# Kernel tuning notes

Measured on AMD Instinct MI355X. Metric: run time of the kernel, lower is better.

The kernel has to match this reference:

```python
import jax, jax.numpy as jnp
import numpy as np
import math

B, T, C = 8, 2048, 1024
KEY_SIZE, VALUE_SIZE = 1024, 1024


def setup_inputs() -> dict:
    key = jax.random.key(0)
    ks = jax.random.split(key, 7)
    s = 1.0 / math.sqrt(C)
    return {
        "input": jax.random.normal(ks[0], (B, T, C), dtype=jnp.float32),
        "mask": jnp.ones((B, T, 1), dtype=jnp.float32),
        "Wq": jax.random.uniform(ks[1], (C, KEY_SIZE), jnp.float32, -s, s),
        "bq": jax.random.uniform(ks[2], (KEY_SIZE,), jnp.float32, -s, s),
        "Wk": jax.random.uniform(ks[3], (C, KEY_SIZE), jnp.float32, -s, s),
        "bk": jax.random.uniform(ks[4], (KEY_SIZE,), jnp.float32, -s, s),
        "Wv": jax.random.uniform(ks[5], (C, VALUE_SIZE), jnp.float32, -s, s),
        "bv": jax.random.uniform(ks[6], (VALUE_SIZE,), jnp.float32, -s, s),
    }


def reference(input, mask, Wq, bq, Wk, bk, Wv, bv):
    # QKV projections: [B, T, C] @ [C, K] -> [B, T, K]
    query = input @ Wq + bq
    keys = input @ Wk + bk
    values = input @ Wv + bv
    # scores[b, tq, tk] = query[b, tq, :] . keys[b, tk, :]
    scores = jnp.einsum("bqk,btk->bqt", query, keys) / math.sqrt(KEY_SIZE)
    # NOTE: softmax over the QUERY dimension (axis=1), as in the original (dim=1)
    attn = jax.nn.softmax(scores, axis=1)
    out = jnp.einsum("bqt,btv->bqv", attn, values)
    return out * mask
```

## Files before the change

kernel.cpp:

```cpp
#include <hip/hip_runtime.h>
#include <hip/hip_bf16.h>
#include <cstdint>

typedef __attribute__((ext_vector_type(8))) __bf16 bf16x8;
typedef __attribute__((ext_vector_type(4))) float f32x4;
typedef __attribute__((ext_vector_type(8))) unsigned short u16x8;

static __device__ __forceinline__ unsigned short f2b(float f) {
    union { float f; unsigned u; } v; v.f = f;
    unsigned r = v.u + 0x7fffu + ((v.u >> 16) & 1u);
    return (unsigned short)(r >> 16);
}
static __device__ __forceinline__ float b2f(unsigned short b) {
    union { unsigned u; float f; } v; v.u = ((unsigned)b) << 16;
    return v.f;
}

#define LL16(g, l) __builtin_amdgcn_global_load_lds( \
    (const __attribute__((address_space(1))) void*)(g), \
    (__attribute__((address_space(3))) void*)(l), 16, 0, 0)

__global__ void conv_f32_bf16(const float* __restrict__ in,
                              unsigned short* __restrict__ out, long n8) {
    long i = (long)blockIdx.x * blockDim.x + threadIdx.x;
    if (i >= n8) return;
    const float4* p = (const float4*)in + i * 2;
    float4 a = p[0], b = p[1];
    u16x8 r;
    r[0] = f2b(a.x); r[1] = f2b(a.y); r[2] = f2b(a.z); r[3] = f2b(a.w);
    r[4] = f2b(b.x); r[5] = f2b(b.y); r[6] = f2b(b.z); r[7] = f2b(b.w);
    *(u16x8*)(out + i * 8) = r;
}

__global__ void transpose_w(const float* __restrict__ w0,
                            const float* __restrict__ w1,
                            const float* __restrict__ w2,
                            unsigned short* __restrict__ out) {
    __shared__ float tile[32][33];
    int z = blockIdx.z;
    const float* W = (z == 0) ? w0 : (z == 1) ? w1 : w2;
    int n0 = blockIdx.x * 32, c0 = blockIdx.y * 32;
    int tx = threadIdx.x & 31, ty = threadIdx.x >> 5;
    #pragma unroll
    for (int i = 0; i < 32; i += 8)
        tile[ty + i][tx] = W[(long)(c0 + ty + i) * 1024 + n0 + tx];
    __syncthreads();
    unsigned short* o = out + (long)z * 1024 * 1024;
    #pragma unroll
    for (int i = 0; i < 32; i += 8)
        o[(long)(n0 + ty + i) * 1024 + c0 + tx] = f2b(tile[tx][ty + i]);
}

__global__ void scale_vt(unsigned short* __restrict__ Vt,
                         const float* __restrict__ colsum) {
    long i8 = ((long)blockIdx.x * 256 + threadIdx.x) * 8;
    int b = (int)(i8 >> 21);
    int rem = (int)(i8 & ((1 << 21) - 1));
    int t = rem & 2047;
    const float* cs = colsum + b * 2048 + t;
    u16x8 v = *(const u16x8*)(Vt + i8);
    u16x8 o;
    #pragma unroll
    for (int j = 0; j < 8; ++j) o[j] = f2b(b2f(v[j]) / cs[j]);
    *(u16x8*)(Vt + i8) = o;
}


#define BAR() __builtin_amdgcn_s_barrier()
#define WAIT_VM2() asm volatile("s_waitcnt vmcnt(2)" ::: "memory")
#define WAIT_VM0() asm volatile("s_waitcnt vmcnt(0)" ::: "memory")

#define STG_A(buf, h, EOFF) do { \
    LL16(((h) ? sA10 : sA00) + (EOFF), ldsA + (buf)*16384 + (h)*8192 + dst0); \
    LL16(((h) ? sA11 : sA01) + (EOFF), ldsA + (buf)*16384 + (h)*8192 + dst1); } while (0)
#define STG_B(buf, h, EOFF) do { \
    LL16(((h) ? sB10 : sB00) + (EOFF), ldsB + (buf)*16384 + (h)*8192 + dst0); \
    LL16(((h) ? sB11 : sB01) + (EOFF), ldsB + (buf)*16384 + (h)*8192 + dst1); } while (0)

#define LDA(d, mh) do { _Pragma("unroll") for (int fi = 0; fi < 4; ++fi) { \
    af[fi][0] = *(const bf16x8*)(ldsA + (d)*16384 + wr*8192 + baA0 + (mh)*4096 + fi*1024); \
    af[fi][1] = *(const bf16x8*)(ldsA + (d)*16384 + wr*8192 + baA1 + (mh)*4096 + fi*1024); } } while (0)
#define LDB(d, nh, BF) do { _Pragma("unroll") for (int fj = 0; fj < 2; ++fj) { \
    BF[fj][0] = *(const bf16x8*)(ldsB + (d)*16384 + wcH*8192 + baB0 + (nh)*2048 + fj*1024); \
    BF[fj][1] = *(const bf16x8*)(ldsB + (d)*16384 + wcH*8192 + baB1 + (nh)*2048 + fj*1024); } } while (0)

#define MMA(mh, nh, BF) do { \
    __builtin_amdgcn_s_setprio(1); \
    _Pragma("unroll") for (int fi = 0; fi < 4; ++fi) \
    _Pragma("unroll") for (int fj = 0; fj < 2; ++fj) { \
        acc[(mh)*4+fi][(nh)*2+fj] = __builtin_amdgcn_mfma_f32_16x16x32_bf16( \
            af[fi][0], BF[fj][0], acc[(mh)*4+fi][(nh)*2+fj], 0, 0, 0); \
        acc[(mh)*4+fi][(nh)*2+fj] = __builtin_amdgcn_mfma_f32_16x16x32_bf16( \
            af[fi][1], BF[fj][1], acc[(mh)*4+fi][(nh)*2+fj], 0, 0, 0); } \
    __builtin_amdgcn_s_setprio(0); } while (0)

template<int MODE>
__global__ __launch_bounds__(512, 2)
void gemm256(const unsigned short* __restrict__ Aall,
             const unsigned short* __restrict__ Ball,
             void* __restrict__ Cv,
             int M, int N, int K, int ldc,
             long aStride, long bStride, long cStride,
             const float* __restrict__ aux, float* __restrict__ colsum) {
    __shared__ unsigned short lds[65536];
    unsigned short* const ldsA = lds;
    unsigned short* const ldsB = lds + 32768;

    const int gx = gridDim.x, gy = gridDim.y;
    const int nxy = gx * gy;
    const int nwg = nxy * gridDim.z;
    const int orig = (blockIdx.z * gy + blockIdx.y) * gx + blockIdx.x;
    const int swz = (orig & 7) * (nwg >> 3) + (orig >> 3);
    const int bz = swz / nxy;
    const int rem = swz - bz * nxy;
    const int by = rem / gx;
    const int bx = rem - by * gx;

    const unsigned short* A  = Aall + (long)bz * aStride;
    const unsigned short* Bt = Ball + (long)bz * bStride;

    const int tid = threadIdx.x;
    const int lane = tid & 63;
    const int w = tid >> 6;
    const int wr = w >> 2, wc = w & 3;
    const int wcH = wc >> 1;
    const int lr = lane & 15, lg = lane >> 4;

    const int bm = by * 256, bn = bx * 256;
    const int NI = K >> 7;

    const int r0 = tid >> 3;
    const int l0 = (tid & 7) ^ (r0 & 7);
    const unsigned short* sA00 = A  + (long)(bm + r0)       * K + l0 * 8;
    const unsigned short* sA01 = A  + (long)(bm + 64 + r0)  * K + l0 * 8;
    const unsigned short* sA10 = A  + (long)(bm + 128 + r0) * K + l0 * 8;
    const unsigned short* sA11 = A  + (long)(bm + 192 + r0) * K + l0 * 8;
    const unsigned short* sB00 = Bt + (long)(bn + r0)       * K + l0 * 8;
    const unsigned short* sB01 = Bt + (long)(bn + 64 + r0)  * K + l0 * 8;
    const unsigned short* sB10 = Bt + (long)(bn + 128 + r0) * K + l0 * 8;
    const unsigned short* sB11 = Bt + (long)(bn + 192 + r0) * K + l0 * 8;
    const int dst0 = w * 512;
    const int dst1 = 4096 + w * 512;

    const int cx0 = (lg ^ (lr & 7)) * 8;
    const int cx1 = ((4 + lg) ^ (lr & 7)) * 8;
    const int baA0 = lr * 64 + cx0;
    const int baA1 = lr * 64 + cx1;
    const int baB0 = ((wc & 1) * 64 + lr) * 64 + cx0;
    const int baB1 = ((wc & 1) * 64 + lr) * 64 + cx1;

    bf16x8 af[4][2], bfA[2][2], bfB[2][2];
    f32x4 acc[8][4] = {};

    STG_B(0, 0, 0); STG_B(0, 1, 0); STG_A(0, 0, 0); STG_A(0, 1, 0);
    STG_B(1, 0, 64);
    WAIT_VM2();
    BAR();

    for (int i = 0; i < NI; ++i) {
        const bool more = (i + 1 < NI);
        LDA(0, 0); LDB(0, 0, bfA); LDB(0, 1, bfB); STG_B(1, 1, 64);
        BAR(); MMA(0, 0, bfA); BAR();

        STG_A(1, 0, 64);
        BAR(); MMA(0, 1, bfB); BAR();

        LDA(0, 1); STG_A(1, 1, 64);
        BAR(); MMA(1, 1, bfB); BAR();

        if (more) STG_B(0, 0, 128);
        BAR(); MMA(1, 0, bfA);
        if (more) { WAIT_VM2(); } else { WAIT_VM0(); }
        BAR();

        LDA(1, 0); LDB(1, 0, bfA); LDB(1, 1, bfB); if (more) STG_B(0, 1, 128);
        BAR(); MMA(0, 0, bfA); BAR();

        if (more) STG_A(0, 0, 128);
        BAR(); MMA(0, 1, bfB); BAR();

        LDA(1, 1); if (more) STG_A(0, 1, 128);
        BAR(); MMA(1, 1, bfB); BAR();

        if (more) STG_B(1, 0, 192);
        BAR(); MMA(1, 0, bfA);
        WAIT_VM2();
        BAR();

        sA00 += 128; sA01 += 128; sA10 += 128; sA11 += 128;
        sB00 += 128; sB01 += 128; sB10 += 128; sB11 += 128;
    }

    const int rloc0 = wr * 128;
    const int cloc0 = wc * 64;

    if (MODE != 3) {
        unsigned short* C = (unsigned short*)Cv + (long)bz * cStride;
        float* cs = colsum + (long)bz * 2048;
        #pragma unroll
        for (int nj = 0; nj < 4; ++nj) {
            int cl = cloc0 + nj * 16 + lr;
            int cb = cl >> 3, cIn = cl & 7;
            float colB = (MODE == 0) ? aux[bn + cl] : 0.f;
            float psum = 0.f;
            #pragma unroll
            for (int mi = 0; mi < 8; ++mi) {
                #pragma unroll
                for (int r = 0; r < 4; ++r) {
                    int rl = rloc0 + mi * 16 + lg * 4 + r;
                    float v = acc[mi][nj][r];
                    if (MODE == 0) v += colB;
                    else if (MODE == 1) v += aux[bm + rl];
                    else { v = __expf(v * 0.03125f); psum += v; }
                    int ch = cb ^ ((rl & 7) << 2);
                    lds[rl * 256 + ch * 8 + cIn] = f2b(v);
                }
            }
            if (MODE == 2) {
                psum += __shfl_xor(psum, 16);
                psum += __shfl_xor(psum, 32);
                if (lg == 0) atomicAdd(&cs[bn + cl], psum);
            }
        }
        BAR();
        #pragma unroll
        for (int it = 0; it < 16; ++it) {
            int lin = it * 512 + tid;
            int row = lin >> 5;
            int c = lin & 31;
            u16x8 v = *(const u16x8*)&lds[row * 256 + ((c ^ ((row & 7) << 2)) << 3)];
            *(u16x8*)&C[(long)(bm + row) * ldc + bn + c * 8] = v;
        }
    } else {
        float* C = (float*)Cv + (long)bz * cStride;
        const float* mk = aux + (long)bz * 2048;
        float* ft = (float*)lds;
        #pragma unroll
        for (int h = 0; h < 2; ++h) {
            if (h) BAR();
            if (wr == h) {
                #pragma unroll
                for (int nj = 0; nj < 4; ++nj) {
                    int cl = cloc0 + nj * 16 + lr;
                    int cf = cl >> 2, cIn = cl & 3;
                    #pragma unroll
                    for (int mi = 0; mi < 8; ++mi) {
                        #pragma unroll
                        for (int r = 0; r < 4; ++r) {
                            int rl = mi * 16 + lg * 4 + r;
                            float m = mk[bm + h * 128 + rl];
                            int cfs = cf ^ ((rl & 7) << 2);
                            ft[rl * 256 + cfs * 4 + cIn] = acc[mi][nj][r] * m;
                        }
                    }
                }
            }
            BAR();
            #pragma unroll
            for (int it = 0; it < 16; ++it) {
                int lin = it * 512 + tid;
                int row = lin >> 6;
                int cf = lin & 63;
                float4 v = *(const float4*)&ft[row * 256 + ((cf ^ ((row & 7) << 2)) << 2)];
                *(float4*)&C[(long)(bm + h * 128 + row) * ldc + bn + cf * 4] = v;
            }
        }
    }
}

extern "C" void kernel_launch(void* const* d_in, const int* in_sizes, int n_in,
                              void* d_out, int out_size, void* d_ws, size_t ws_size,
                              hipStream_t stream) {
    const float* x    = (const float*)d_in[0];
    const float* mask = (const float*)d_in[1];
    const float* Wq   = (const float*)d_in[2];
    const float* bq   = (const float*)d_in[3];
    const float* Wk   = (const float*)d_in[4];
    const float* bk   = (const float*)d_in[5];
    const float* Wv   = (const float*)d_in[6];
    const float* bv   = (const float*)d_in[7];
    float* out = (float*)d_out;

    const long MT = 16384;
    unsigned short* Xb = (unsigned short*)d_ws;
    unsigned short* Wt = Xb + MT * 1024;
    unsigned short* Q  = Wt + 3L * 1024 * 1024;
    unsigned short* Kk = Q  + MT * 1024;
    unsigned short* Vt = Kk + MT * 1024;
    unsigned short* E  = Vt + 8L * 1024 * 2048;
    float* colsum = (float*)(E + 8L * 2048 * 2048);
    size_t need = (size_t)((char*)(colsum + 8 * 2048) - (char*)d_ws);
    if (ws_size < need) return;

    conv_f32_bf16<<<(MT * 1024) / 8 / 256, 256, 0, stream>>>(x, Xb, (MT * 1024) / 8);
    transpose_w<<<dim3(32, 32, 3), 256, 0, stream>>>(Wq, Wk, Wv, Wt);
    gemm256<0><<<dim3(4, 64, 1), 512, 0, stream>>>(
        Xb, Wt, Q, 16384, 1024, 1024, 1024, 0, 0, 0, bq, nullptr);
    gemm256<0><<<dim3(4, 64, 1), 512, 0, stream>>>(
        Xb, Wt + 1048576, Kk, 16384, 1024, 1024, 1024, 0, 0, 0, bk, nullptr);
    gemm256<1><<<dim3(8, 4, 8), 512, 0, stream>>>(
        Wt + 2097152, Xb, Vt, 1024, 2048, 1024, 2048,
        0, 2048L * 1024, 1024L * 2048, bv, nullptr);
    hipMemsetAsync(colsum, 0, 8 * 2048 * sizeof(float), stream);
    gemm256<2><<<dim3(8, 8, 8), 512, 0, stream>>>(
        Q, Kk, E, 2048, 2048, 1024, 2048,
        2048L * 1024, 2048L * 1024, 2048L * 2048, nullptr, colsum);
    scale_vt<<<8192, 256, 0, stream>>>(Vt, colsum);
    gemm256<3><<<dim3(4, 8, 8), 512, 0, stream>>>(
        E, Vt, out, 2048, 1024, 2048, 1024,
        2048L * 2048, 1024L * 2048, 2048L * 1024, mask, nullptr);
}
```

Measured before the change: 309.9 us.

## Restructure GEMM main loop to overlap LDS reads with MFMA and cut barriers

```diff
diff --git a/kernel.cpp b/kernel.cpp
--- a/kernel.cpp
+++ b/kernel.cpp
@@ -68,6 +68,7 @@
 
 #define BAR() __builtin_amdgcn_s_barrier()
 #define WAIT_VM2() asm volatile("s_waitcnt vmcnt(2)" ::: "memory")
+#define WAIT_VM1() asm volatile("s_waitcnt vmcnt(1)" ::: "memory")
 #define WAIT_VM0() asm volatile("s_waitcnt vmcnt(0)" ::: "memory")
 
 #define STG_A(buf, h, EOFF) do { \
@@ -152,39 +153,35 @@
     bf16x8 af[4][2], bfA[2][2], bfB[2][2];
     f32x4 acc[8][4] = {};
 
-    STG_B(0, 0, 0); STG_B(0, 1, 0); STG_A(0, 0, 0); STG_A(0, 1, 0);
-    STG_B(1, 0, 64);
-    WAIT_VM2();
+    STG_A(0, 0, 0); STG_A(0, 1, 0);
+    STG_B(0, 0, 0); STG_B(0, 1, 0);
+    STG_B(1, 0, 64); STG_B(1, 1, 64);
+    WAIT_VM0();
     BAR();
+    LDA(0, 0);
+    LDB(0, 0, bfA);
+    LDB(0, 1, bfB);
 
     for (int i = 0; i < NI; ++i) {
         const bool more = (i + 1 < NI);
-        LDA(0, 0); LDB(0, 0, bfA); LDB(0, 1, bfB); STG_B(1, 1, 64);
-        BAR(); MMA(0, 0, bfA); BAR();
-
-        STG_A(1, 0, 64);
-        BAR(); MMA(0, 1, bfB); BAR();
-
-        LDA(0, 1); STG_A(1, 1, 64);
-        BAR(); MMA(1, 1, bfB); BAR();
-
-        if (more) STG_B(0, 0, 128);
-        BAR(); MMA(1, 0, bfA);
-        if (more) { WAIT_VM2(); } else { WAIT_VM0(); }
-        BAR();
-
-        LDA(1, 0); LDB(1, 0, bfA); LDB(1, 1, bfB); if (more) STG_B(0, 1, 128);
-        BAR(); MMA(0, 0, bfA); BAR();
-
-        if (more) STG_A(0, 0, 128);
-        BAR(); MMA(0, 1, bfB); BAR();
-
-        LDA(1, 1); if (more) STG_A(0, 1, 128);
-        BAR(); MMA(1, 1, bfB); BAR();
-
-        if (more) STG_B(1, 0, 192);
-        BAR(); MMA(1, 0, bfA);
-        WAIT_VM2();
+        MMA(0, 0, bfA); STG_A(1, 0, 64);
+        BAR();
+        MMA(0, 1, bfB); LDA(0, 1); STG_A(1, 1, 64);
+        WAIT_VM2(); BAR();
+        MMA(1, 1, bfB); LDB(1, 1, bfB); if (more) STG_B(0, 0, 128);
+        if (more) { WAIT_VM1(); } else { WAIT_VM0(); }
+        BAR();
+        MMA(1, 0, bfA); LDB(1, 0, bfA); LDA(1, 0); if (more) STG_B(0, 1, 128);
+        BAR();
+
+        MMA(0, 0, bfA); if (more) STG_A(0, 0, 128);
+        BAR();
+        MMA(0, 1, bfB); LDA(1, 1); if (more) STG_A(0, 1, 128);
+        WAIT_VM2(); BAR();
+        MMA(1, 1, bfB); if (more) { LDB(0, 1, bfB); STG_B(1, 0, 192); }
+        if (more) { WAIT_VM1(); } else { WAIT_VM0(); }
+        BAR();
+        MMA(1, 0, bfA); if (more) { LDB(0, 0, bfA); LDA(0, 0); STG_B(1, 1, 192); }
         BAR();
 
         sA00 += 128; sA01 += 128; sA10 += 128; sA11 += 128;
```

New measurement: 303.9 us. No clear change (-1.9%).

## Replace 256x256 GEMM tile with 256x128 tile using 32x32 MFMA

Applied to the files above, without the earlier changes.

```diff
diff --git a/kernel.cpp b/kernel.cpp
--- a/kernel.cpp
+++ b/kernel.cpp
@@ -3,7 +3,7 @@
 #include <cstdint>
 
 typedef __attribute__((ext_vector_type(8))) __bf16 bf16x8;
-typedef __attribute__((ext_vector_type(4))) float f32x4;
+typedef __attribute__((ext_vector_type(16))) float f32x16;
 typedef __attribute__((ext_vector_type(8))) unsigned short u16x8;
 
 static __device__ __forceinline__ unsigned short f2b(float f) {
@@ -19,6 +19,9 @@
 #define LL16(g, l) __builtin_amdgcn_global_load_lds( \
     (const __attribute__((address_space(1))) void*)(g), \
     (__attribute__((address_space(3))) void*)(l), 16, 0, 0)
+
+#define BAR() __builtin_amdgcn_s_barrier()
+#define WAIT_VM0() asm volatile("s_waitcnt vmcnt(0)" ::: "memory")
 
 __global__ void conv_f32_bf16(const float* __restrict__ in,
                               unsigned short* __restrict__ out, long n8) {
@@ -66,45 +69,17 @@
 }
 
 
-#define BAR() __builtin_amdgcn_s_barrier()
-#define WAIT_VM2() asm volatile("s_waitcnt vmcnt(2)" ::: "memory")
-#define WAIT_VM0() asm volatile("s_waitcnt vmcnt(0)" ::: "memory")
-
-#define STG_A(buf, h, EOFF) do { \
-    LL16(((h) ? sA10 : sA00) + (EOFF), ldsA + (buf)*16384 + (h)*8192 + dst0); \
-    LL16(((h) ? sA11 : sA01) + (EOFF), ldsA + (buf)*16384 + (h)*8192 + dst1); } while (0)
-#define STG_B(buf, h, EOFF) do { \
-    LL16(((h) ? sB10 : sB00) + (EOFF), ldsB + (buf)*16384 + (h)*8192 + dst0); \
-    LL16(((h) ? sB11 : sB01) + (EOFF), ldsB + (buf)*16384 + (h)*8192 + dst1); } while (0)
-
-#define LDA(d, mh) do { _Pragma("unroll") for (int fi = 0; fi < 4; ++fi) { \
-    af[fi][0] = *(const bf16x8*)(ldsA + (d)*16384 + wr*8192 + baA0 + (mh)*4096 + fi*1024); \
-    af[fi][1] = *(const bf16x8*)(ldsA + (d)*16384 + wr*8192 + baA1 + (mh)*4096 + fi*1024); } } while (0)
-#define LDB(d, nh, BF) do { _Pragma("unroll") for (int fj = 0; fj < 2; ++fj) { \
-    BF[fj][0] = *(const bf16x8*)(ldsB + (d)*16384 + wcH*8192 + baB0 + (nh)*2048 + fj*1024); \
-    BF[fj][1] = *(const bf16x8*)(ldsB + (d)*16384 + wcH*8192 + baB1 + (nh)*2048 + fj*1024); } } while (0)
-
-#define MMA(mh, nh, BF) do { \
-    __builtin_amdgcn_s_setprio(1); \
-    _Pragma("unroll") for (int fi = 0; fi < 4; ++fi) \
-    _Pragma("unroll") for (int fj = 0; fj < 2; ++fj) { \
-        acc[(mh)*4+fi][(nh)*2+fj] = __builtin_amdgcn_mfma_f32_16x16x32_bf16( \
-            af[fi][0], BF[fj][0], acc[(mh)*4+fi][(nh)*2+fj], 0, 0, 0); \
-        acc[(mh)*4+fi][(nh)*2+fj] = __builtin_amdgcn_mfma_f32_16x16x32_bf16( \
-            af[fi][1], BF[fj][1], acc[(mh)*4+fi][(nh)*2+fj], 0, 0, 0); } \
-    __builtin_amdgcn_s_setprio(0); } while (0)
-
 template<int MODE>
-__global__ __launch_bounds__(512, 2)
-void gemm256(const unsigned short* __restrict__ Aall,
+__global__ __launch_bounds__(512, 4)
+void gemm128(const unsigned short* __restrict__ Aall,
              const unsigned short* __restrict__ Ball,
              void* __restrict__ Cv,
              int M, int N, int K, int ldc,
              long aStride, long bStride, long cStride,
              const float* __restrict__ aux, float* __restrict__ colsum) {
-    __shared__ unsigned short lds[65536];
+    __shared__ unsigned short lds[32768];
     unsigned short* const ldsA = lds;
-    unsigned short* const ldsB = lds + 32768;
+    unsigned short* const ldsB = lds + 16384;
 
     const int gx = gridDim.x, gy = gridDim.y;
     const int nxy = gx * gy;
@@ -122,113 +97,98 @@
     const int tid = threadIdx.x;
     const int lane = tid & 63;
     const int w = tid >> 6;
-    const int wr = w >> 2, wc = w & 3;
-    const int wcH = wc >> 1;
-    const int lr = lane & 15, lg = lane >> 4;
-
-    const int bm = by * 256, bn = bx * 256;
-    const int NI = K >> 7;
-
-    const int r0 = tid >> 3;
-    const int l0 = (tid & 7) ^ (r0 & 7);
-    const unsigned short* sA00 = A  + (long)(bm + r0)       * K + l0 * 8;
-    const unsigned short* sA01 = A  + (long)(bm + 64 + r0)  * K + l0 * 8;
-    const unsigned short* sA10 = A  + (long)(bm + 128 + r0) * K + l0 * 8;
-    const unsigned short* sA11 = A  + (long)(bm + 192 + r0) * K + l0 * 8;
-    const unsigned short* sB00 = Bt + (long)(bn + r0)       * K + l0 * 8;
-    const unsigned short* sB01 = Bt + (long)(bn + 64 + r0)  * K + l0 * 8;
-    const unsigned short* sB10 = Bt + (long)(bn + 128 + r0) * K + l0 * 8;
-    const unsigned short* sB11 = Bt + (long)(bn + 192 + r0) * K + l0 * 8;
-    const int dst0 = w * 512;
-    const int dst1 = 4096 + w * 512;
-
-    const int cx0 = (lg ^ (lr & 7)) * 8;
-    const int cx1 = ((4 + lg) ^ (lr & 7)) * 8;
-    const int baA0 = lr * 64 + cx0;
-    const int baA1 = lr * 64 + cx1;
-    const int baB0 = ((wc & 1) * 64 + lr) * 64 + cx0;
-    const int baB1 = ((wc & 1) * 64 + lr) * 64 + cx1;
-
-    bf16x8 af[4][2], bfA[2][2], bfB[2][2];
-    f32x4 acc[8][4] = {};
-
-    STG_B(0, 0, 0); STG_B(0, 1, 0); STG_A(0, 0, 0); STG_A(0, 1, 0);
-    STG_B(1, 0, 64);
-    WAIT_VM2();
+    const int wrow = w >> 1, wcol = w & 1;
+    const int l31 = lane & 31, hi = lane >> 5;
+
+    const int bm = by * 256, bn = bx * 128;
+    const int NT = K >> 5;
+
+    const int r0 = tid >> 2;
+    const int c0 = (tid & 3) ^ (r0 & 3);
+    const unsigned short* sA0 = A  + (long)(bm + r0)       * K + c0 * 8;
+    const unsigned short* sA1 = A  + (long)(bm + 128 + r0) * K + c0 * 8;
+    const unsigned short* sB0 = Bt + (long)(bn + r0)       * K + c0 * 8;
+    const int dA0 = w * 512;
+    const int dA1 = 4096 + w * 512;
+    const int dB0 = w * 512;
+
+    const int s3 = l31 & 3;
+    const int cx0 = ((0 + hi) ^ s3) * 8;
+    const int cx1 = ((2 + hi) ^ s3) * 8;
+    const int baA = (wrow * 64 + l31) * 32;
+    const int baB = (wcol * 64 + l31) * 32;
+
+    f32x16 acc[2][2] = {};
+
+    LL16(sA0, ldsA + dA0); LL16(sA1, ldsA + dA1); LL16(sB0, ldsB + dB0);
+    WAIT_VM0();
     BAR();
 
-    for (int i = 0; i < NI; ++i) {
-        const bool more = (i + 1 < NI);
-        LDA(0, 0); LDB(0, 0, bfA); LDB(0, 1, bfB); STG_B(1, 1, 64);
-        BAR(); MMA(0, 0, bfA); BAR();
-
-        STG_A(1, 0, 64);
-        BAR(); MMA(0, 1, bfB); BAR();
-
-        LDA(0, 1); STG_A(1, 1, 64);
-        BAR(); MMA(1, 1, bfB); BAR();
-
-        if (more) STG_B(0, 0, 128);
-        BAR(); MMA(1, 0, bfA);
-        if (more) { WAIT_VM2(); } else { WAIT_VM0(); }
+    for (int t = 0; t < NT; ++t) {
+        const int buf = t & 1, nbuf = buf ^ 1;
+        if (t + 1 < NT) {
+            const long ko = (long)(t + 1) * 32;
+            LL16(sA0 + ko, ldsA + nbuf * 8192 + dA0);
+            LL16(sA1 + ko, ldsA + nbuf * 8192 + dA1);
+            LL16(sB0 + ko, ldsB + nbuf * 4096 + dB0);
+        }
+        bf16x8 a00 = *(const bf16x8*)(ldsA + buf * 8192 + baA + 0    + cx0);
+        bf16x8 a01 = *(const bf16x8*)(ldsA + buf * 8192 + baA + 0    + cx1);
+        bf16x8 a10 = *(const bf16x8*)(ldsA + buf * 8192 + baA + 1024 + cx0);
+        bf16x8 a11 = *(const bf16x8*)(ldsA + buf * 8192 + baA + 1024 + cx1);
+        bf16x8 b00 = *(const bf16x8*)(ldsB + buf * 4096 + baB + 0    + cx0);
+        bf16x8 b01 = *(const bf16x8*)(ldsB + buf * 4096 + baB + 0    + cx1);
+        bf16x8 b10 = *(const bf16x8*)(ldsB + buf * 4096 + baB + 1024 + cx0);
+        bf16x8 b11 = *(const bf16x8*)(ldsB + buf * 4096 + baB + 1024 + cx1);
+
+        __builtin_amdgcn_s_setprio(1);
+        acc[0][0] = __builtin_amdgcn_mfma_f32_32x32x16_bf16(a00, b00, acc[0][0], 0, 0, 0);
+        acc[1][0] = __builtin_amdgcn_mfma_f32_32x32x16_bf16(a10, b00, acc[1][0], 0, 0, 0);
+        acc[0][1] = __builtin_amdgcn_mfma_f32_32x32x16_bf16(a00, b10, acc[0][1], 0, 0, 0);
+        acc[1][1] = __builtin_amdgcn_mfma_f32_32x32x16_bf16(a10, b10, acc[1][1], 0, 0, 0);
+        acc[0][0] = __builtin_amdgcn_mfma_f32_32x32x16_bf16(a01, b01, acc[0][0], 0, 0, 0);
+        acc[1][0] = __builtin_amdgcn_mfma_f32_32x32x16_bf16(a11, b01, acc[1][0], 0, 0, 0);
+        acc[0][1] = __builtin_amdgcn_mfma_f32_32x32x16_bf16(a01, b11, acc[0][1], 0, 0, 0);
+        acc[1][1] = __builtin_amdgcn_mfma_f32_32x32x16_bf16(a11, b11, acc[1][1], 0, 0, 0);
+        __builtin_amdgcn_s_setprio(0);
+
+        WAIT_VM0();
         BAR();
-
-        LDA(1, 0); LDB(1, 0, bfA); LDB(1, 1, bfB); if (more) STG_B(0, 1, 128);
-        BAR(); MMA(0, 0, bfA); BAR();
-
-        if (more) STG_A(0, 0, 128);
-        BAR(); MMA(0, 1, bfB); BAR();
-
-        LDA(1, 1); if (more) STG_A(0, 1, 128);
-        BAR(); MMA(1, 1, bfB); BAR();
-
-        if (more) STG_B(1, 0, 192);
-        BAR(); MMA(1, 0, bfA);
-        WAIT_VM2();
-        BAR();
-
-        sA00 += 128; sA01 += 128; sA10 += 128; sA11 += 128;
-        sB00 += 128; sB01 += 128; sB10 += 128; sB11 += 128;
     }
-
-    const int rloc0 = wr * 128;
-    const int cloc0 = wc * 64;
 
     if (MODE != 3) {
         unsigned short* C = (unsigned short*)Cv + (long)bz * cStride;
         float* cs = colsum + (long)bz * 2048;
         #pragma unroll
-        for (int nj = 0; nj < 4; ++nj) {
-            int cl = cloc0 + nj * 16 + lr;
-            int cb = cl >> 3, cIn = cl & 7;
+        for (int nj = 0; nj < 2; ++nj) {
+            const int cl = wcol * 64 + nj * 32 + l31;
+            const int cb = cl >> 3, cIn = cl & 7;
             float colB = (MODE == 0) ? aux[bn + cl] : 0.f;
             float psum = 0.f;
             #pragma unroll
-            for (int mi = 0; mi < 8; ++mi) {
+            for (int mi = 0; mi < 2; ++mi) {
                 #pragma unroll
-                for (int r = 0; r < 4; ++r) {
-                    int rl = rloc0 + mi * 16 + lg * 4 + r;
-                    float v = acc[mi][nj][r];
+                for (int rg = 0; rg < 16; ++rg) {
+                    const int rl = wrow * 64 + mi * 32 + (rg & 3) + ((rg >> 2) << 3) + (hi << 2);
+                    float v = acc[mi][nj][rg];
                     if (MODE == 0) v += colB;
                     else if (MODE == 1) v += aux[bm + rl];
                     else { v = __expf(v * 0.03125f); psum += v; }
-                    int ch = cb ^ ((rl & 7) << 2);
-                    lds[rl * 256 + ch * 8 + cIn] = f2b(v);
+                    lds[rl * 128 + ((cb ^ ((rl & 7) << 1)) << 3) + cIn] = f2b(v);
                 }
             }
             if (MODE == 2) {
-                psum += __shfl_xor(psum, 16);
                 psum += __shfl_xor(psum, 32);
-                if (lg == 0) atomicAdd(&cs[bn + cl], psum);
+                if (hi == 0) atomicAdd(&cs[bn + cl], psum);
             }
         }
         BAR();
         #pragma unroll
-        for (int it = 0; it < 16; ++it) {
+        for (int it = 0; it < 8; ++it) {
             int lin = it * 512 + tid;
-            int row = lin >> 5;
-            int c = lin & 31;
-            u16x8 v = *(const u16x8*)&lds[row * 256 + ((c ^ ((row & 7) << 2)) << 3)];
+            int row = lin >> 4;
+            int c = lin & 15;
+            u16x8 v = *(const u16x8*)&lds[row * 128 + ((c ^ ((row & 7) << 1)) << 3)];
             *(u16x8*)&C[(long)(bm + row) * ldc + bn + c * 8] = v;
         }
     } else {
@@ -238,30 +198,30 @@
         #pragma unroll
         for (int h = 0; h < 2; ++h) {
             if (h) BAR();
-            if (wr == h) {
+            if ((wrow >> 1) == h) {
                 #pragma unroll
-                for (int nj = 0; nj < 4; ++nj) {
-                    int cl = cloc0 + nj * 16 + lr;
-                    int cf = cl >> 2, cIn = cl & 3;
+                for (int nj = 0; nj < 2; ++nj) {
+                    const int cl = wcol * 64 + nj * 32 + l31;
+                    const int cf = cl >> 2, cIn = cl & 3;
                     #pragma unroll
-                    for (int mi = 0; mi < 8; ++mi) {
+                    for (int mi = 0; mi < 2; ++mi) {
                         #pragma unroll
-                        for (int r = 0; r < 4; ++r) {
-                            int rl = mi * 16 + lg * 4 + r;
-                            float m = mk[bm + h * 128 + rl];
-                            int cfs = cf ^ ((rl & 7) << 2);
-                            ft[rl * 256 + cfs * 4 + cIn] = acc[mi][nj][r] * m;
+                        for (int rg = 0; rg < 16; ++rg) {
+                            const int rl2 = (wrow & 1) * 64 + mi * 32 + (rg & 3) + ((rg >> 2) << 3) + (hi << 2);
+                            const int gr = bm + h * 128 + rl2;
+                            ft[rl2 * 128 + ((cf ^ ((rl2 & 7) << 2)) << 2) + cIn] =
+                                acc[mi][nj][rg] * mk[gr];
                         }
                     }
                 }
             }
             BAR();
             #pragma unroll
-            for (int it = 0; it < 16; ++it) {
+            for (int it = 0; it < 8; ++it) {
                 int lin = it * 512 + tid;
-                int row = lin >> 6;
-                int cf = lin & 63;
-                float4 v = *(const float4*)&ft[row * 256 + ((cf ^ ((row & 7) << 2)) << 2)];
+                int row = lin >> 5;
+                int cf = lin & 31;
+                float4 v = *(const float4*)&ft[row * 128 + ((cf ^ ((row & 7) << 2)) << 2)];
                 *(float4*)&C[(long)(bm + h * 128 + row) * ldc + bn + cf * 4] = v;
             }
         }
@@ -294,19 +254,19 @@
 
     conv_f32_bf16<<<(MT * 1024) / 8 / 256, 256, 0, stream>>>(x, Xb, (MT * 1024) / 8);
     transpose_w<<<dim3(32, 32, 3), 256, 0, stream>>>(Wq, Wk, Wv, Wt);
-    gemm256<0><<<dim3(4, 64, 1), 512, 0, stream>>>(
+    gemm128<0><<<dim3(8, 64, 1), 512, 0, stream>>>(
         Xb, Wt, Q, 16384, 1024, 1024, 1024, 0, 0, 0, bq, nullptr);
-    gemm256<0><<<dim3(4, 64, 1), 512, 0, stream>>>(
+    gemm128<0><<<dim3(8, 64, 1), 512, 0, stream>>>(
         Xb, Wt + 1048576, Kk, 16384, 1024, 1024, 1024, 0, 0, 0, bk, nullptr);
-    gemm256<1><<<dim3(8, 4, 8), 512, 0, stream>>>(
+    gemm128<1><<<dim3(16, 4, 8), 512, 0, stream>>>(
         Wt + 2097152, Xb, Vt, 1024, 2048, 1024, 2048,
         0, 2048L * 1024, 1024L * 2048, bv, nullptr);
     hipMemsetAsync(colsum, 0, 8 * 2048 * sizeof(float), stream);
-    gemm256<2><<<dim3(8, 8, 8), 512, 0, stream>>>(
+    gemm128<2><<<dim3(16, 8, 8), 512, 0, stream>>>(
         Q, Kk, E, 2048, 2048, 1024, 2048,
         2048L * 1024, 2048L * 1024, 2048L * 2048, nullptr, colsum);
     scale_vt<<<8192, 256, 0, stream>>>(Vt, colsum);
-    gemm256<3><<<dim3(4, 8, 8), 512, 0, stream>>>(
+    gemm128<3><<<dim3(8, 8, 8), 512, 0, stream>>>(
         E, Vt, out, 2048, 1024, 2048, 1024,
         2048L * 2048, 1024L * 2048, 2048L * 1024, mask, nullptr);
 }
```

After: 375.0 us. 21.0% more time.
